# Performance work log

Hardware: AMD Instinct MI355X
Metric: run time of the kernel (lower is better)

The kernel has to match this reference:

```python
import jax, jax.numpy as jnp
import numpy as np

B, HS, WS = 4, 64, 64
UP = 8
H, W = HS * UP, WS * UP
C_ORI, C_MNT, C_OFF = 90, 180, 8
K = 1024            # max minutiae candidates per image (64*64 cells max 4096)
THRESH = 0.5
DIST_T = 16.0
ANG_T = np.pi / 6


def setup_inputs() -> dict:
    key = jax.random.key(0)
    ks = jax.random.split(key, 8)
    return {
        'segmentation': jax.random.uniform(ks[0], (B, 1, HS, WS), jnp.float32),
        'segmentation_up': jax.random.uniform(ks[1], (B, 1, H, W), jnp.float32),
        'orientation_up': jax.random.normal(ks[2], (B, C_ORI, H, W), jnp.float32),
        'enhanced_real': jax.random.normal(ks[3], (B, 1, H, W), jnp.float32),
        'minutiae_score': jax.random.uniform(ks[4], (B, 1, HS, WS), jnp.float32),
        'minutiae_orientation': jax.random.normal(ks[5], (B, C_MNT, HS, WS), jnp.float32),
        'minutiae_x_offset': jax.random.normal(ks[6], (B, C_OFF, HS, WS), jnp.float32),
        'minutiae_y_offset': jax.random.normal(ks[7], (B, C_OFF, HS, WS), jnp.float32),
    }


def _opening(x, k):
    # morphological opening (erosion then dilation) with a k x k ones kernel,
    # separable min/max pooling; geodesic border (pad so border is neutral).
    pl, pr = (k - 1) // 2, k // 2

    def pool(v, comp, init, pad_val):
        vp = jnp.pad(v, ((0, 0), (pl, pr), (pl, pr)), constant_values=pad_val)
        vp = jax.lax.reduce_window(vp, init, comp, (1, k, 1), (1, 1, 1), 'VALID')
        return jax.lax.reduce_window(vp, init, comp, (1, 1, k), (1, 1, 1), 'VALID')

    er = pool(x, jax.lax.min, np.inf, 1e4)
    return pool(er, jax.lax.max, -np.inf, -1e4)


def _nms_keep(xy, ang, valid):
    # xy: [K,2], ang: [K], valid: [K] bool; entries already sorted by score desc
    d = jnp.sqrt(jnp.sum((xy[:, None, :] - xy[None, :, :]) ** 2, axis=-1))
    da = jnp.abs(ang[:, None] - ang[None, :])
    da = jnp.minimum(da, 2 * jnp.pi - da)
    sup = (d < DIST_T) & (da < ANG_T) & valid[:, None] & valid[None, :]
    idxs = jnp.arange(K)

    def body(i, keep):
        return keep & ~(sup[i] & (idxs > i) & keep[i])

    return jax.lax.fori_loop(0, K, body, valid)


def _detect(score, ori, xo, yo):
    # score: [HS,WS]; ori: [C_MNT,HS,WS]; xo/yo: [C_OFF,HS,WS]
    h, w = score.shape
    flat = score.reshape(-1)
    masked = jnp.where(flat > THRESH, flat, -1.0)
    vals, idx = jax.lax.top_k(masked, K)          # sorted descending
    valid = vals > THRESH
    rows = idx // w
    cols = idx % w
    ang_idx = jnp.argmax(ori.reshape(C_MNT, -1)[:, idx], axis=0)
    xoff = jnp.argmax(xo.reshape(C_OFF, -1)[:, idx], axis=0)
    yoff = jnp.argmax(yo.reshape(C_OFF, -1)[:, idx], axis=0)
    angles = (ang_idx.astype(jnp.float32) * 2.0 - 89.0) * (np.pi / 180.0)
    xc = cols.astype(jnp.float32) * 8.0 + xoff.astype(jnp.float32)
    yc = rows.astype(jnp.float32) * 8.0 + yoff.astype(jnp.float32)
    scores = flat[idx]
    m = jnp.stack([xc, yc, angles, scores], axis=-1)  # [K,4]
    keep = _nms_keep(m[:, :2], angles, valid)
    return m, keep


def reference(segmentation, segmentation_up, orientation_up, enhanced_real,
              minutiae_score, minutiae_orientation, minutiae_x_offset,
              minutiae_y_offset):
    mask = _opening(jnp.round(segmentation[:, 0]), 5)          # [B,HS,WS]
    mask_up = _opening(jnp.round(segmentation_up[:, 0]), 5 * UP)  # [B,H,W]

    score = minutiae_score[:, 0] * mask
    minut, keep = jax.vmap(_detect)(score, minutiae_orientation,
                                    minutiae_x_offset, minutiae_y_offset)
    minut = minut * keep[..., None].astype(minut.dtype)       # zero suppressed

    ori_field = (jnp.argmax(orientation_up, axis=1).astype(jnp.float32) * 2.0
                 - 90.0) * (np.pi / 180.0) * mask_up

    enh = enhanced_real[:, 0] * mask_up
    ef = enh.reshape(B, -1)
    emin = ef.min(axis=1, keepdims=True)
    emax = ef.max(axis=1, keepdims=True)
    enh_vis = ((ef - emin) / (emax - emin + 1e-8)).reshape(B, H, W) * 255.0

    return (minut, keep.astype(jnp.float32), enh_vis, mask_up * 255.0, ori_field)
```

## Files before the change

kernel.cpp:

```cpp
#include <hip/hip_runtime.h>
#include <math.h>

#define HSd 64
#define WSd 64
#define Hh 512
#define Wh 512
#define Bn 4
#define C_ORIc 90
#define C_MNTc 180
#define C_OFFc 8
#define Kc 1024

#define O_MINUT 0
#define O_KEEP  (Bn*Kc*4)
#define O_VIS   (O_KEEP + Bn*Kc)
#define O_MASK  (O_VIS + Bn*Hh*Wh)
#define O_ORI   (O_MASK + Bn*Hh*Wh)

#define PI_180 0.017453292519943295f
#define TWO_PI 6.283185307179586f
#define ANG_T  0.5235987755982988f

template <bool ISMIN, bool BIN>
__global__ __launch_bounds__(256) void pass_v(const float* __restrict__ in,
                                              float* __restrict__ out)
{
    int c = blockIdx.x * 64 + threadIdx.x;
    int r = blockIdx.y * 4 + threadIdx.y;
    int b = blockIdx.z;
    const float* p = in + (size_t)b * Hh * Wh;
    int lo = max(r - 19, 0), hi = min(r + 20, Hh - 1);
    float acc = ISMIN ? 1e30f : -1e30f;
    for (int rr = lo; rr <= hi; rr++) {
        float v = p[rr * Wh + c];
        if (BIN) v = rintf(v);
        acc = ISMIN ? fminf(acc, v) : fmaxf(acc, v);
    }
    out[(size_t)b * Hh * Wh + (size_t)r * Wh + c] = acc;
}

template <bool ISMIN>
__global__ __launch_bounds__(256) void pass_h(const float* __restrict__ in,
                                              float* __restrict__ out)
{
    int c = blockIdx.x * 64 + threadIdx.x;
    int r = blockIdx.y * 4 + threadIdx.y;
    int b = blockIdx.z;
    const float* p = in + (size_t)b * Hh * Wh + (size_t)r * Wh;
    int lo = max(c - 19, 0), hi = min(c + 20, Wh - 1);
    float acc = ISMIN ? 1e30f : -1e30f;
    for (int cc = lo; cc <= hi; cc++)
        acc = ISMIN ? fminf(acc, p[cc]) : fmaxf(acc, p[cc]);
    out[(size_t)b * Hh * Wh + (size_t)r * Wh + c] = acc;
}

__global__ __launch_bounds__(512) void final_up_kernel(const float* __restrict__ vmx,
                                                       const float* __restrict__ ori,
                                                       const float* __restrict__ enh,
                                                       float* __restrict__ out,
                                                       float* __restrict__ partials)
{
    int r = blockIdx.x, b = blockIdx.y, c = threadIdx.x;
    __shared__ float row[512];
    __shared__ float rmn[512];
    __shared__ float rmx[512];
    size_t base = (size_t)b * Hh * Wh + (size_t)r * Wh;
    row[c] = vmx[base + c];
    __syncthreads();
    int lo = max(c - 19, 0), hi = min(c + 20, Wh - 1);
    float m = -1e30f;
    for (int cc = lo; cc <= hi; cc++) m = fmaxf(m, row[cc]);
    out[O_MASK + base + c] = m * 255.0f;

    float of = 0.0f;
    if (m != 0.0f) {
        const float* op = ori + (size_t)b * C_ORIc * Hh * Wh + (size_t)r * Wh + c;
        float best = op[0];
        int bi = 0;
        for (int ch = 1; ch < C_ORIc; ch++) {
            float v = op[(size_t)ch * Hh * Wh];
            if (v > best) { best = v; bi = ch; }
        }
        of = ((float)bi * 2.0f - 90.0f) * PI_180 * m;
    }
    out[O_ORI + base + c] = of;

    float e = enh[base + c] * m;
    rmn[c] = e; rmx[c] = e;
    __syncthreads();
    for (int s2 = 256; s2 > 0; s2 >>= 1) {
        if (c < s2) {
            rmn[c] = fminf(rmn[c], rmn[c + s2]);
            rmx[c] = fmaxf(rmx[c], rmx[c + s2]);
        }
        __syncthreads();
    }
    if (c == 0) {
        partials[(b * Hh + r) * 2 + 0] = rmn[0];
        partials[(b * Hh + r) * 2 + 1] = rmx[0];
    }
}

__global__ __launch_bounds__(512) void reduce_mm_kernel(const float* __restrict__ partials,
                                                        float* __restrict__ mm)
{
    int b = blockIdx.x, t = threadIdx.x;
    __shared__ float mn[512];
    __shared__ float mx[512];
    mn[t] = partials[(b * 512 + t) * 2 + 0];
    mx[t] = partials[(b * 512 + t) * 2 + 1];
    __syncthreads();
    for (int s = 256; s > 0; s >>= 1) {
        if (t < s) {
            mn[t] = fminf(mn[t], mn[t + s]);
            mx[t] = fmaxf(mx[t], mx[t + s]);
        }
        __syncthreads();
    }
    if (t == 0) { mm[b * 2] = mn[0]; mm[b * 2 + 1] = mx[0]; }
}

__global__ __launch_bounds__(256) void vis_kernel(const float* __restrict__ enh,
                                                  const float* __restrict__ maskout,
                                                  const float* __restrict__ mm,
                                                  float* __restrict__ vis)
{
    int idx = blockIdx.x * 256 + threadIdx.x;
    int b = idx >> 18;
    float m = (maskout[idx] != 0.0f) ? 1.0f : 0.0f;
    float e = enh[idx] * m;
    float emin = mm[b * 2], emax = mm[b * 2 + 1];
    float r = (e - emin) / (emax - emin + 1e-8f);
    vis[idx] = r * 255.0f;
}

__global__ __launch_bounds__(1024) void detect_kernel(const float* __restrict__ mscore,
                                                      const float* __restrict__ seg,
                                                      const float* __restrict__ mo,
                                                      const float* __restrict__ xo,
                                                      const float* __restrict__ yo,
                                                      float* __restrict__ out)
{
    int b = blockIdx.x;
    int tid = threadIdx.x;
    __shared__ unsigned long long keys[4096];
    __shared__ float maskT[64][65];
    float* scratch = (float*)keys;

    const float* sg = seg + b * 4096;
    for (int i = tid; i < 4096; i += 1024)
        maskT[i >> 6][i & 63] = rintf(sg[i]);
    __syncthreads();
    for (int i = tid; i < 4096; i += 1024) {
        int r = i >> 6, c = i & 63;
        int lo = max(r - 2, 0), hi = min(r + 2, 63);
        float m = 1e30f;
        for (int rr = lo; rr <= hi; rr++) m = fminf(m, maskT[rr][c]);
        scratch[r * 65 + c] = m;
    }
    __syncthreads();
    for (int i = tid; i < 4096; i += 1024) {
        int r = i >> 6, c = i & 63;
        int lo = max(c - 2, 0), hi = min(c + 2, 63);
        float m = 1e30f;
        for (int cc = lo; cc <= hi; cc++) m = fminf(m, scratch[r * 65 + cc]);
        maskT[r][c] = m;
    }
    __syncthreads();
    for (int i = tid; i < 4096; i += 1024) {
        int r = i >> 6, c = i & 63;
        int lo = max(r - 2, 0), hi = min(r + 2, 63);
        float m = -1e30f;
        for (int rr = lo; rr <= hi; rr++) m = fmaxf(m, maskT[rr][c]);
        scratch[r * 65 + c] = m;
    }
    __syncthreads();
    for (int i = tid; i < 4096; i += 1024) {
        int r = i >> 6, c = i & 63;
        int lo = max(c - 2, 0), hi = min(c + 2, 63);
        float m = -1e30f;
        for (int cc = lo; cc <= hi; cc++) m = fmaxf(m, scratch[r * 65 + cc]);
        maskT[r][c] = m;
    }
    __syncthreads();

    const float* sp = mscore + b * 4096;
    bool anyv = false;
    for (int i = tid; i < 4096; i += 1024) {
        float s = sp[i] * maskT[i >> 6][i & 63];
        anyv |= (s > 0.5f);
    }
    if (!__syncthreads_or(anyv)) {
        float* mout = out + O_MINUT + (size_t)b * Kc * 4 + (size_t)tid * 4;
        mout[0] = 0.f; mout[1] = 0.f; mout[2] = 0.f; mout[3] = 0.f;
        out[O_KEEP + b * Kc + tid] = 0.f;
        return;
    }

    for (int i = tid; i < 4096; i += 1024) {
        float s = sp[i] * maskT[i >> 6][i & 63];
        float mval = (s > 0.5f) ? s : -1.0f;
        unsigned int fb = __float_as_uint(mval);
        unsigned int od = (fb & 0x80000000u) ? ~fb : (fb | 0x80000000u);
        keys[i] = ((unsigned long long)(~od) << 32) | (unsigned int)i;
    }
    for (int k = 2; k <= 4096; k <<= 1) {
        for (int j = k >> 1; j > 0; j >>= 1) {
            __syncthreads();
            for (int t = tid; t < 4096; t += 1024) {
                int ixj = t ^ j;
                if (ixj > t) {
                    unsigned long long va = keys[t], vb = keys[ixj];
                    bool up = ((t & k) == 0);
                    if ((va > vb) == up) { keys[t] = vb; keys[ixj] = va; }
                }
            }
        }
    }
    __syncthreads();

    int idx = (int)(keys[tid] & 0xffffffffu);
    float s = sp[idx] * maskT[idx >> 6][idx & 63];
    bool valid = s > 0.5f;
    int Nv = __syncthreads_count(valid);

    float* sx = scratch;
    float* sy = scratch + 1024;
    float* sa = scratch + 2048;
    int*   keep = (int*)(scratch + 3072);

    float xc = 0.f, yc = 0.f, ang = 0.f;
    if (tid < Nv) {
        int rr = idx >> 6, cc = idx & 63;
        const float* op = mo + (size_t)b * C_MNTc * 4096 + idx;
        float best = op[0]; int bi = 0;
        for (int ch = 1; ch < C_MNTc; ch++) {
            float v = op[ch * 4096];
            if (v > best) { best = v; bi = ch; }
        }
        const float* xp = xo + (size_t)b * C_OFFc * 4096 + idx;
        float bxv = xp[0]; int bx = 0;
        for (int ch = 1; ch < C_OFFc; ch++) {
            float v = xp[ch * 4096];
            if (v > bxv) { bxv = v; bx = ch; }
        }
        const float* yp = yo + (size_t)b * C_OFFc * 4096 + idx;
        float byv = yp[0]; int by = 0;
        for (int ch = 1; ch < C_OFFc; ch++) {
            float v = yp[ch * 4096];
            if (v > byv) { byv = v; by = ch; }
        }
        ang = ((float)bi * 2.0f - 89.0f) * PI_180;
        xc = (float)cc * 8.0f + (float)bx;
        yc = (float)rr * 8.0f + (float)by;
        sx[tid] = xc; sy[tid] = yc; sa[tid] = ang;
        keep[tid] = 1;
    } else {
        keep[tid] = 0;
    }
    __syncthreads();

    for (int i = 0; i < Nv; i++) {
        if (keep[i] && tid > i && tid < Nv && keep[tid]) {
            float dx = sx[tid] - sx[i], dy = sy[tid] - sy[i];
            float d = sqrtf(dx * dx + dy * dy);
            float da = fabsf(sa[tid] - sa[i]);
            da = fminf(da, TWO_PI - da);
            if (d < 16.0f && da < ANG_T) keep[tid] = 0;
        }
        __syncthreads();
    }

    int kf = keep[tid];
    float* mout = out + O_MINUT + (size_t)b * Kc * 4 + (size_t)tid * 4;
    if (kf) {
        mout[0] = xc; mout[1] = yc; mout[2] = ang; mout[3] = s;
    } else {
        mout[0] = 0.f; mout[1] = 0.f; mout[2] = 0.f; mout[3] = 0.f;
    }
    out[O_KEEP + b * Kc + tid] = (float)kf;
}

extern "C" void kernel_launch(void* const* d_in, const int* in_sizes, int n_in,
                              void* d_out_, int out_size, void* d_ws, size_t ws_size,
                              hipStream_t stream)
{
    const float* seg    = (const float*)d_in[0];
    const float* segup  = (const float*)d_in[1];
    const float* oriup  = (const float*)d_in[2];
    const float* enh    = (const float*)d_in[3];
    const float* mscore = (const float*)d_in[4];
    const float* mori   = (const float*)d_in[5];
    const float* mxo    = (const float*)d_in[6];
    const float* myo    = (const float*)d_in[7];
    float* out = (float*)d_out_;

    float* partials = (float*)d_ws;
    float* mm       = partials + Bn * 512 * 2;

    float* T1 = out + O_VIS;
    float* T2 = out + O_ORI;

    detect_kernel<<<Bn, 1024, 0, stream>>>(mscore, seg, mori, mxo, myo, out);

    dim3 pb(64, 4);
    dim3 pg(8, 128, Bn);
    pass_v<true, true><<<pg, pb, 0, stream>>>(segup, T1);
    pass_h<true><<<pg, pb, 0, stream>>>(T1, T2);
    pass_v<false, false><<<pg, pb, 0, stream>>>(T2, T1);
    final_up_kernel<<<dim3(Hh, Bn), 512, 0, stream>>>(T1, oriup, enh, out, partials);
    reduce_mm_kernel<<<Bn, 512, 0, stream>>>(partials, mm);
    vis_kernel<<<(Bn * Hh * Wh) / 256, 256, 0, stream>>>(enh, out + O_MASK, mm, out + O_VIS);
}
```

Measured before the change: 511.8 us.

## Bit-pack upsampled mask and do 40x40 opening with bitwise ops in detect kernel

The upsampled segmentation is binarized into 32-bit words, and the 40x40 erosion and dilation run as bitwise AND/OR with doubling shifts inside the per-image detect kernel, replacing three float window passes over global memory. The final and vis kernels read mask bits from workspace, and the per-row min/max partials are combined with atomics on order-preserving encoded floats, which removes the separate reduction kernel. The cost is that the opening now runs on only 4 blocks, serialized ahead of the detection work, which may limit parallelism. The diff also adds a full horizontal dilation pass that the old code left to the final kernel.

New measurement: 533.6 us. +4.3%, slower.

```diff
diff --git a/kernel.cpp b/kernel.cpp
--- a/kernel.cpp
+++ b/kernel.cpp
@@ -1,8 +1,6 @@
 #include <hip/hip_runtime.h>
 #include <math.h>
 
-#define HSd 64
-#define WSd 64
 #define Hh 512
 #define Wh 512
 #define Bn 4
@@ -21,131 +19,130 @@
 #define TWO_PI 6.283185307179586f
 #define ANG_T  0.5235987755982988f
 
-template <bool ISMIN, bool BIN>
-__global__ __launch_bounds__(256) void pass_v(const float* __restrict__ in,
-                                              float* __restrict__ out)
-{
-    int c = blockIdx.x * 64 + threadIdx.x;
-    int r = blockIdx.y * 4 + threadIdx.y;
-    int b = blockIdx.z;
-    const float* p = in + (size_t)b * Hh * Wh;
-    int lo = max(r - 19, 0), hi = min(r + 20, Hh - 1);
-    float acc = ISMIN ? 1e30f : -1e30f;
-    for (int rr = lo; rr <= hi; rr++) {
-        float v = p[rr * Wh + c];
-        if (BIN) v = rintf(v);
-        acc = ISMIN ? fminf(acc, v) : fmaxf(acc, v);
-    }
-    out[(size_t)b * Hh * Wh + (size_t)r * Wh + c] = acc;
-}
-
-template <bool ISMIN>
-__global__ __launch_bounds__(256) void pass_h(const float* __restrict__ in,
-                                              float* __restrict__ out)
-{
-    int c = blockIdx.x * 64 + threadIdx.x;
-    int r = blockIdx.y * 4 + threadIdx.y;
-    int b = blockIdx.z;
-    const float* p = in + (size_t)b * Hh * Wh + (size_t)r * Wh;
-    int lo = max(c - 19, 0), hi = min(c + 20, Wh - 1);
-    float acc = ISMIN ? 1e30f : -1e30f;
-    for (int cc = lo; cc <= hi; cc++)
-        acc = ISMIN ? fminf(acc, p[cc]) : fmaxf(acc, p[cc]);
-    out[(size_t)b * Hh * Wh + (size_t)r * Wh + c] = acc;
-}
-
-__global__ __launch_bounds__(512) void final_up_kernel(const float* __restrict__ vmx,
-                                                       const float* __restrict__ ori,
-                                                       const float* __restrict__ enh,
-                                                       float* __restrict__ out,
-                                                       float* __restrict__ partials)
-{
-    int r = blockIdx.x, b = blockIdx.y, c = threadIdx.x;
-    __shared__ float row[512];
-    __shared__ float rmn[512];
-    __shared__ float rmx[512];
-    size_t base = (size_t)b * Hh * Wh + (size_t)r * Wh;
-    row[c] = vmx[base + c];
-    __syncthreads();
-    int lo = max(c - 19, 0), hi = min(c + 20, Wh - 1);
-    float m = -1e30f;
-    for (int cc = lo; cc <= hi; cc++) m = fmaxf(m, row[cc]);
-    out[O_MASK + base + c] = m * 255.0f;
-
-    float of = 0.0f;
-    if (m != 0.0f) {
-        const float* op = ori + (size_t)b * C_ORIc * Hh * Wh + (size_t)r * Wh + c;
-        float best = op[0];
-        int bi = 0;
-        for (int ch = 1; ch < C_ORIc; ch++) {
-            float v = op[(size_t)ch * Hh * Wh];
-            if (v > best) { best = v; bi = ch; }
-        }
-        of = ((float)bi * 2.0f - 90.0f) * PI_180 * m;
-    }
-    out[O_ORI + base + c] = of;
-
-    float e = enh[base + c] * m;
-    rmn[c] = e; rmx[c] = e;
-    __syncthreads();
-    for (int s2 = 256; s2 > 0; s2 >>= 1) {
-        if (c < s2) {
-            rmn[c] = fminf(rmn[c], rmn[c + s2]);
-            rmx[c] = fmaxf(rmx[c], rmx[c + s2]);
-        }
-        __syncthreads();
-    }
-    if (c == 0) {
-        partials[(b * Hh + r) * 2 + 0] = rmn[0];
-        partials[(b * Hh + r) * 2 + 1] = rmx[0];
-    }
-}
-
-__global__ __launch_bounds__(512) void reduce_mm_kernel(const float* __restrict__ partials,
-                                                        float* __restrict__ mm)
-{
-    int b = blockIdx.x, t = threadIdx.x;
-    __shared__ float mn[512];
-    __shared__ float mx[512];
-    mn[t] = partials[(b * 512 + t) * 2 + 0];
-    mx[t] = partials[(b * 512 + t) * 2 + 1];
-    __syncthreads();
-    for (int s = 256; s > 0; s >>= 1) {
-        if (t < s) {
-            mn[t] = fminf(mn[t], mn[t + s]);
-            mx[t] = fmaxf(mx[t], mx[t + s]);
-        }
-        __syncthreads();
-    }
-    if (t == 0) { mm[b * 2] = mn[0]; mm[b * 2 + 1] = mx[0]; }
-}
-
-__global__ __launch_bounds__(256) void vis_kernel(const float* __restrict__ enh,
-                                                  const float* __restrict__ maskout,
-                                                  const float* __restrict__ mm,
-                                                  float* __restrict__ vis)
-{
-    int idx = blockIdx.x * 256 + threadIdx.x;
-    int b = idx >> 18;
-    float m = (maskout[idx] != 0.0f) ? 1.0f : 0.0f;
-    float e = enh[idx] * m;
-    float emin = mm[b * 2], emax = mm[b * 2 + 1];
-    float r = (e - emin) / (emax - emin + 1e-8f);
-    vis[idx] = r * 255.0f;
-}
-
-__global__ __launch_bounds__(1024) void detect_kernel(const float* __restrict__ mscore,
-                                                      const float* __restrict__ seg,
-                                                      const float* __restrict__ mo,
-                                                      const float* __restrict__ xo,
-                                                      const float* __restrict__ yo,
-                                                      float* __restrict__ out)
+#define WS_BITS 0
+#define WS_MM   (Bn*8192)
+
+__device__ __forceinline__ unsigned enc_f(float f) {
+    unsigned u = __float_as_uint(f);
+    return (u & 0x80000000u) ? ~u : (u | 0x80000000u);
+}
+__device__ __forceinline__ float dec_f(unsigned e) {
+    return __uint_as_float((e & 0x80000000u) ? (e ^ 0x80000000u) : ~e);
+}
+
+template <bool ER>
+__device__ void pass_vert(unsigned* A, unsigned* T, int tid) {
+    const unsigned F = ER ? 0xFFFFFFFFu : 0u;
+    for (int i = tid; i < 8192; i += 1024) {
+        int r = i >> 4;
+        unsigned v = A[i];
+        unsigned a1 = (r + 1 < 512) ? A[i + 16] : F;
+        unsigned a2 = (r + 2 < 512) ? A[i + 32] : F;
+        unsigned a3 = (r + 3 < 512) ? A[i + 48] : F;
+        unsigned a4 = (r + 4 < 512) ? A[i + 64] : F;
+        T[i] = ER ? (v & a1 & a2 & a3 & a4) : (v | a1 | a2 | a3 | a4);
+    }
+    __syncthreads();
+    for (int i = tid; i < 8192; i += 1024) {
+        int r = i >> 4;
+        unsigned b1 = (r + 5 < 512) ? T[i + 80] : F;
+        A[i] = ER ? (T[i] & b1) : (T[i] | b1);
+    }
+    __syncthreads();
+    for (int i = tid; i < 8192; i += 1024) {
+        int r = i >> 4;
+        unsigned b1 = (r + 10 < 512) ? A[i + 160] : F;
+        T[i] = ER ? (A[i] & b1) : (A[i] | b1);
+    }
+    __syncthreads();
+    for (int i = tid; i < 8192; i += 1024) {
+        int r = i >> 4;
+        unsigned a = (r >= 19) ? T[i - 304] : F;
+        unsigned c = (r + 1 < 512) ? T[i + 16] : F;
+        A[i] = ER ? (a & c) : (a | c);
+    }
+    __syncthreads();
+}
+
+template <bool ER>
+__device__ void pass_horz(unsigned* A, unsigned* T, int tid) {
+    const unsigned F = ER ? 0xFFFFFFFFu : 0u;
+    for (int i = tid; i < 8192; i += 1024) {
+        int w = i & 15;
+        unsigned lo = A[i], hi = (w < 15) ? A[i + 1] : F;
+        unsigned v = lo;
+        unsigned s1 = (lo >> 1) | (hi << 31);
+        unsigned s2 = (lo >> 2) | (hi << 30);
+        unsigned s3 = (lo >> 3) | (hi << 29);
+        unsigned s4 = (lo >> 4) | (hi << 28);
+        T[i] = ER ? (v & s1 & s2 & s3 & s4) : (v | s1 | s2 | s3 | s4);
+    }
+    __syncthreads();
+    for (int i = tid; i < 8192; i += 1024) {
+        int w = i & 15;
+        unsigned lo = T[i], hi = (w < 15) ? T[i + 1] : F;
+        unsigned s5 = (lo >> 5) | (hi << 27);
+        A[i] = ER ? (lo & s5) : (lo | s5);
+    }
+    __syncthreads();
+    for (int i = tid; i < 8192; i += 1024) {
+        int w = i & 15;
+        unsigned lo = A[i], hi = (w < 15) ? A[i + 1] : F;
+        unsigned s10 = (lo >> 10) | (hi << 22);
+        T[i] = ER ? (lo & s10) : (lo | s10);
+    }
+    __syncthreads();
+    for (int i = tid; i < 8192; i += 1024) {
+        int w = i & 15;
+        unsigned lo = T[i];
+        unsigned hi = (w < 15) ? T[i + 1] : F;
+        unsigned lom = (w > 0) ? T[i - 1] : F;
+        unsigned a = (lo << 19) | (lom >> 13);
+        unsigned c = (lo >> 1) | (hi << 31);
+        A[i] = ER ? (a & c) : (a | c);
+    }
+    __syncthreads();
+}
+
+__global__ __launch_bounds__(1024) void detect_open_kernel(
+    const float* __restrict__ mscore, const float* __restrict__ seg,
+    const float* __restrict__ segup, const float* __restrict__ mo,
+    const float* __restrict__ xo, const float* __restrict__ yo,
+    float* __restrict__ out, unsigned* __restrict__ ws)
 {
     int b = blockIdx.x;
     int tid = threadIdx.x;
     __shared__ unsigned long long keys[4096];
+    __shared__ unsigned T[8192];
     __shared__ float maskT[64][65];
+    unsigned* A = (unsigned*)keys;
     float* scratch = (float*)keys;
+
+    if (tid == 0) { ws[WS_MM + b * 2] = 0xFFFFFFFFu; ws[WS_MM + b * 2 + 1] = 0u; }
+
+    const float* p = segup + (size_t)b * Hh * Wh;
+    for (int w = tid; w < 8192; w += 1024) {
+        const float4* q = (const float4*)(p + w * 32);
+        unsigned bits = 0;
+        #pragma unroll
+        for (int j = 0; j < 8; j++) {
+            float4 v = q[j];
+            bits |= ((unsigned)(v.x > 0.5f)) << (4 * j + 0);
+            bits |= ((unsigned)(v.y > 0.5f)) << (4 * j + 1);
+            bits |= ((unsigned)(v.z > 0.5f)) << (4 * j + 2);
+            bits |= ((unsigned)(v.w > 0.5f)) << (4 * j + 3);
+        }
+        A[w] = bits;
+    }
+    __syncthreads();
+
+    pass_vert<true>(A, T, tid);
+    pass_horz<true>(A, T, tid);
+    pass_vert<false>(A, T, tid);
+    pass_horz<false>(A, T, tid);
+
+    for (int i = tid; i < 8192; i += 1024) ws[WS_BITS + b * 8192 + i] = A[i];
+    __syncthreads();
 
     const float* sg = seg + b * 4096;
     for (int i = tid; i < 4096; i += 1024)
@@ -200,9 +197,9 @@
     for (int i = tid; i < 4096; i += 1024) {
         float s = sp[i] * maskT[i >> 6][i & 63];
         float mval = (s > 0.5f) ? s : -1.0f;
-        unsigned int fb = __float_as_uint(mval);
-        unsigned int od = (fb & 0x80000000u) ? ~fb : (fb | 0x80000000u);
-        keys[i] = ((unsigned long long)(~od) << 32) | (unsigned int)i;
+        unsigned fb = __float_as_uint(mval);
+        unsigned od = (fb & 0x80000000u) ? ~fb : (fb | 0x80000000u);
+        keys[i] = ((unsigned long long)(~od) << 32) | (unsigned)i;
     }
     for (int k = 2; k <= 4096; k <<= 1) {
         for (int j = k >> 1; j > 0; j >>= 1) {
@@ -232,10 +229,10 @@
     float xc = 0.f, yc = 0.f, ang = 0.f;
     if (tid < Nv) {
         int rr = idx >> 6, cc = idx & 63;
-        const float* op = mo + (size_t)b * C_MNTc * 4096 + idx;
-        float best = op[0]; int bi = 0;
+        const float* op_ = mo + (size_t)b * C_MNTc * 4096 + idx;
+        float best = op_[0]; int bi = 0;
         for (int ch = 1; ch < C_MNTc; ch++) {
-            float v = op[ch * 4096];
+            float v = op_[ch * 4096];
             if (v > best) { best = v; bi = ch; }
         }
         const float* xp = xo + (size_t)b * C_OFFc * 4096 + idx;
@@ -279,6 +276,63 @@
         mout[0] = 0.f; mout[1] = 0.f; mout[2] = 0.f; mout[3] = 0.f;
     }
     out[O_KEEP + b * Kc + tid] = (float)kf;
+}
+
+__global__ __launch_bounds__(512) void fused_final_kernel(
+    const unsigned* __restrict__ ws, const float* __restrict__ ori,
+    const float* __restrict__ enh, float* __restrict__ out,
+    unsigned* __restrict__ mmu)
+{
+    int r = blockIdx.x, b = blockIdx.y, c = threadIdx.x;
+    __shared__ float rmn[512];
+    __shared__ float rmx[512];
+    size_t base = (size_t)b * Hh * Wh + (size_t)r * Wh;
+    unsigned word = ws[WS_BITS + b * 8192 + r * 16 + (c >> 5)];
+    float m = (float)((word >> (c & 31)) & 1u);
+    out[O_MASK + base + c] = m * 255.0f;
+
+    float of = 0.0f;
+    if (m != 0.0f) {
+        const float* op_ = ori + (size_t)b * C_ORIc * Hh * Wh + (size_t)r * Wh + c;
+        float best = op_[0];
+        int bi = 0;
+        for (int ch = 1; ch < C_ORIc; ch++) {
+            float v = op_[(size_t)ch * Hh * Wh];
+            if (v > best) { best = v; bi = ch; }
+        }
+        of = ((float)bi * 2.0f - 90.0f) * PI_180 * m;
+    }
+    out[O_ORI + base + c] = of;
+
+    float e = enh[base + c] * m;
+    rmn[c] = e; rmx[c] = e;
+    __syncthreads();
+    for (int s = 256; s > 0; s >>= 1) {
+        if (c < s) {
+            rmn[c] = fminf(rmn[c], rmn[c + s]);
+            rmx[c] = fmaxf(rmx[c], rmx[c + s]);
+        }
+        __syncthreads();
+    }
+    if (c == 0) {
+        atomicMin(&mmu[b * 2 + 0], enc_f(rmn[0]));
+        atomicMax(&mmu[b * 2 + 1], enc_f(rmx[0]));
+    }
+}
+
+__global__ __launch_bounds__(256) void vis_kernel(
+    const float* __restrict__ enh, const unsigned* __restrict__ ws,
+    float* __restrict__ out)
+{
+    int idx = blockIdx.x * 256 + threadIdx.x;
+    int b = idx >> 18;
+    int pix = idx & 0x3FFFF;
+    unsigned word = ws[WS_BITS + b * 8192 + (pix >> 5)];
+    float m = (float)((word >> (pix & 31)) & 1u);
+    float e = enh[idx] * m;
+    float emin = dec_f(ws[WS_MM + b * 2 + 0]);
+    float emax = dec_f(ws[WS_MM + b * 2 + 1]);
+    out[O_VIS + idx] = (e - emin) / (emax - emin + 1e-8f) * 255.0f;
 }
 
 extern "C" void kernel_launch(void* const* d_in, const int* in_sizes, int n_in,
@@ -294,21 +348,11 @@
     const float* mxo    = (const float*)d_in[6];
     const float* myo    = (const float*)d_in[7];
     float* out = (float*)d_out_;
-
-    float* partials = (float*)d_ws;
-    float* mm       = partials + Bn * 512 * 2;
-
-    float* T1 = out + O_VIS;
-    float* T2 = out + O_ORI;
-
-    detect_kernel<<<Bn, 1024, 0, stream>>>(mscore, seg, mori, mxo, myo, out);
-
-    dim3 pb(64, 4);
-    dim3 pg(8, 128, Bn);
-    pass_v<true, true><<<pg, pb, 0, stream>>>(segup, T1);
-    pass_h<true><<<pg, pb, 0, stream>>>(T1, T2);
-    pass_v<false, false><<<pg, pb, 0, stream>>>(T2, T1);
-    final_up_kernel<<<dim3(Hh, Bn), 512, 0, stream>>>(T1, oriup, enh, out, partials);
-    reduce_mm_kernel<<<Bn, 512, 0, stream>>>(partials, mm);
-    vis_kernel<<<(Bn * Hh * Wh) / 256, 256, 0, stream>>>(enh, out + O_MASK, mm, out + O_VIS);
-}
+    unsigned* ws = (unsigned*)d_ws;
+
+    detect_open_kernel<<<Bn, 1024, 0, stream>>>(mscore, seg, segup, mori, mxo,
+                                                myo, out, ws);
+    fused_final_kernel<<<dim3(Hh, Bn), 512, 0, stream>>>(ws, oriup, enh, out,
+                                                         ws + WS_MM);
+    vis_kernel<<<(Bn * Hh * Wh) / 256, 256, 0, stream>>>(enh, ws, out);
+}
```
